# Kernel optimization log

Measured on AMD Instinct MI355X. Metric: run time of the kernel, lower is better.

The kernel has to match this reference:

```python
import jax, jax.numpy as jnp
import numpy as np

LN_EPS = 1e-12  # BERT LayerNorm eps


def _lstm_dir(x, wih, whh, bih, bhh, reverse):
    # x: [T, B, D] -> outputs [T, B, Hd]; torch gate order i, f, g, o
    B = x.shape[1]
    Hd = whh.shape[1]
    b = bih + bhh

    def step(carry, xt):
        h, c = carry
        gates = xt @ wih.T + h @ whh.T + b  # [B, 4*Hd]
        i, f, g, o = jnp.split(gates, 4, axis=-1)
        c = jax.nn.sigmoid(f) * c + jax.nn.sigmoid(i) * jnp.tanh(g)
        h = jax.nn.sigmoid(o) * jnp.tanh(c)
        return (h, c), h

    init = (jnp.zeros((B, Hd), x.dtype), jnp.zeros((B, Hd), x.dtype))
    _, ys = jax.lax.scan(step, init, x, reverse=reverse)
    return ys


def _forward(input_ids, labels, word_emb, pos_emb, type_emb, ln_g, ln_b,
             w_ih, w_hh, b_ih, b_hh, fc_w, fc_b, crf_start, crf_end, crf_trans):
    B, T = input_ids.shape
    # BERT embeddings (eval mode: dropout = identity)
    emb = word_emb[input_ids] + pos_emb[:T][None, :, :] + type_emb[0][None, None, :]
    mu = emb.mean(-1, keepdims=True)
    var = ((emb - mu) ** 2).mean(-1, keepdims=True)
    emb = (emb - mu) / jnp.sqrt(var + LN_EPS) * ln_g + ln_b

    # stacked bidirectional LSTM
    x = emb.transpose(1, 0, 2)  # [T, B, 768]
    n_layers = w_ih.shape[0]
    for l in range(n_layers):
        f = _lstm_dir(x, w_ih[l, 0], w_hh[l, 0], b_ih[l, 0], b_hh[l, 0], False)
        r = _lstm_dir(x, w_ih[l, 1], w_hh[l, 1], b_ih[l, 1], b_hh[l, 1], True)
        x = jnp.concatenate([f, r], axis=-1)  # [T, B, 768]
    out = x.transpose(1, 0, 2)  # [B, T, 768]

    em = out @ fc_w.T + fc_b  # emissions [B, T, C]

    # CRF log-likelihood (full mask, torchcrf reduction='sum')
    gold_em = jnp.take_along_axis(em, labels[..., None], axis=2)[..., 0]  # [B, T]
    score = (crf_start[labels[:, 0]]
             + gold_em.sum(axis=1)
             + crf_trans[labels[:, :-1], labels[:, 1:]].sum(axis=1)
             + crf_end[labels[:, -1]])

    alpha0 = crf_start[None, :] + em[:, 0]  # [B, C]

    def step(alpha, e_t):
        a = jax.nn.logsumexp(alpha[:, :, None] + crf_trans[None, :, :], axis=1) + e_t
        return a, None

    alpha, _ = jax.lax.scan(step, alpha0, em[:, 1:].transpose(1, 0, 2))
    logZ = jax.nn.logsumexp(alpha + crf_end[None, :], axis=1)  # [B]
    return jnp.sum(logZ - score)  # loss = -llh


def setup_inputs() -> dict:
    key = jax.random.key(0)
    ks = jax.random.split(key, 16)
    B, T, V, P, D, C, L, Hd = 32, 256, 30522, 512, 768, 14, 2, 384
    s = 0.05
    return {
        "input_ids": jax.random.randint(ks[0], (B, T), 0, V),
        "labels": jax.random.randint(ks[1], (B, T), 0, C),
        "word_emb": jax.random.normal(ks[2], (V, D), jnp.float32) * 0.02,
        "pos_emb": jax.random.normal(ks[3], (P, D), jnp.float32) * 0.02,
        "type_emb": jax.random.normal(ks[4], (2, D), jnp.float32) * 0.02,
        "ln_g": jnp.ones((D,), jnp.float32),
        "ln_b": jnp.zeros((D,), jnp.float32),
        "w_ih": jax.random.normal(ks[5], (L, 2, 4 * Hd, D), jnp.float32) * s,
        "w_hh": jax.random.normal(ks[6], (L, 2, 4 * Hd, Hd), jnp.float32) * s,
        "b_ih": jax.random.normal(ks[7], (L, 2, 4 * Hd), jnp.float32) * s,
        "b_hh": jax.random.normal(ks[8], (L, 2, 4 * Hd), jnp.float32) * s,
        "fc_w": jax.random.normal(ks[9], (C, D), jnp.float32) * s,
        "fc_b": jnp.zeros((C,), jnp.float32),
        "crf_start": jax.random.normal(ks[10], (C,), jnp.float32) * 0.1,
        "crf_end": jax.random.normal(ks[11], (C,), jnp.float32) * 0.1,
        "crf_trans": jax.random.normal(ks[12], (C, C), jnp.float32) * 0.1,
    }


def reference(input_ids, labels, word_emb, pos_emb, type_emb, ln_g, ln_b,
              w_ih, w_hh, b_ih, b_hh, fc_w, fc_b, crf_start, crf_end, crf_trans):
    return _forward(input_ids, labels, word_emb, pos_emb, type_emb, ln_g, ln_b,
                    w_ih, w_hh, b_ih, b_hh, fc_w, fc_b, crf_start, crf_end, crf_trans)
```

## Files before the change

### kernel.cpp

```cpp
#include <hip/hip_runtime.h>

typedef unsigned short u16;
typedef unsigned long long u64;
typedef __bf16 bfx8 __attribute__((ext_vector_type(8)));
typedef float  fx4  __attribute__((ext_vector_type(4)));

static __device__ __forceinline__ float b2f(u16 u){
  unsigned v = ((unsigned)u) << 16;
  return __builtin_bit_cast(float, v);
}
static __device__ __forceinline__ u16 f2b(float f){
  unsigned u = __builtin_bit_cast(unsigned, f);
  u = (u + 0x7FFFu + ((u >> 16) & 1u)) >> 16;
  return (u16)u;
}
static __device__ __forceinline__ float blo(unsigned v){ return b2f((u16)(v & 0xFFFFu)); }
static __device__ __forceinline__ float bhi(unsigned v){ return b2f((u16)(v >> 16)); }
static __device__ __forceinline__ float sigm(float x){
  float cx = fminf(fmaxf(x, -30.f), 30.f);
  float e = __expf(-cx);
  return __builtin_amdgcn_rcpf(1.f + e);
}
static __device__ __forceinline__ float tanh_f(float x){
  float cx = fminf(fmaxf(x, -15.f), 15.f);
  float e = __expf(2.f * cx);
  return (e - 1.f) * __builtin_amdgcn_rcpf(e + 1.f);
}
static __device__ __forceinline__ u64 ald64(const u64* p){
  return __hip_atomic_load(p, __ATOMIC_RELAXED, __HIP_MEMORY_SCOPE_AGENT);
}
static __device__ __forceinline__ void ast64(u64* p, u64 v){
  __hip_atomic_store(p, v, __ATOMIC_RELAXED, __HIP_MEMORY_SCOPE_AGENT);
}

__global__ __launch_bounds__(256) void embed_ln(
    const int* __restrict__ ids, const float* __restrict__ we,
    const float* __restrict__ pe, const float* __restrict__ te,
    const float* __restrict__ lng, const float* __restrict__ lnb,
    u16* __restrict__ X)
{
  int row = blockIdx.x;
  int t = row >> 5, b = row & 31;
  int id = ids[b * 256 + t];
  int tid = threadIdx.x;
  int wv = tid >> 6, lane = tid & 63;
  __shared__ float red[8];
  float v[3]; float s = 0.f, s2 = 0.f;
  const float* wrow = we + (long)id * 768;
  const float* prow = pe + (long)t * 768;
#pragma unroll
  for (int u = 0; u < 3; ++u){
    int k = tid + 256 * u;
    float x = wrow[k] + prow[k] + te[k];
    v[u] = x; s += x; s2 += x * x;
  }
#pragma unroll
  for (int o = 32; o > 0; o >>= 1){ s += __shfl_xor(s, o); s2 += __shfl_xor(s2, o); }
  if (lane == 0){ red[wv] = s; red[4 + wv] = s2; }
  __syncthreads();
  float S  = red[0] + red[1] + red[2] + red[3];
  float S2 = red[4] + red[5] + red[6] + red[7];
  float mu = S * (1.f / 768.f);
  float var = S2 * (1.f / 768.f) - mu * mu;
  float rs = rsqrtf(var + 1e-12f);
#pragma unroll
  for (int u = 0; u < 3; ++u){
    int k = tid + 256 * u;
    float y = (v[u] - mu) * rs * lng[k] + lnb[k];
    X[(long)row * 768 + k] = f2b(y);
  }
}

__global__ __launch_bounds__(256) void gemm_pre(
    const u16* __restrict__ A,
    const float* __restrict__ W,
    const float* __restrict__ bi,
    const float* __restrict__ bh,
    u16* __restrict__ pre)
{
  __shared__ u16 la[64][40];
  __shared__ u16 lb[64][40];
  int m0 = blockIdx.x * 64, n0 = blockIdx.y * 64;
  int tid = threadIdx.x;
  int wv = tid >> 6, lane = tid & 63;
  int l15 = lane & 15, l4 = lane >> 4;
  int r = tid >> 2, seg = (tid & 3) * 8;
  fx4 acc[4];
#pragma unroll
  for (int i = 0; i < 4; ++i){ acc[i][0]=0.f; acc[i][1]=0.f; acc[i][2]=0.f; acc[i][3]=0.f; }
  for (int k0 = 0; k0 < 768; k0 += 32){
    __syncthreads();
    *reinterpret_cast<uint4*>(&la[r][seg]) =
        *reinterpret_cast<const uint4*>(&A[(long)(m0 + r) * 768 + k0 + seg]);
    {
      const float* src = &W[(long)(n0 + r) * 768 + k0 + seg];
      union { u16 h[8]; uint4 v; } tb;
#pragma unroll
      for (int e = 0; e < 8; ++e) tb.h[e] = f2b(src[e]);
      *reinterpret_cast<uint4*>(&lb[r][seg]) = tb.v;
    }
    __syncthreads();
    bfx8 af = __builtin_bit_cast(bfx8, *reinterpret_cast<const uint4*>(&la[wv * 16 + l15][8 * l4]));
#pragma unroll
    for (int nt = 0; nt < 4; ++nt){
      bfx8 bf = __builtin_bit_cast(bfx8, *reinterpret_cast<const uint4*>(&lb[nt * 16 + l15][8 * l4]));
      acc[nt] = __builtin_amdgcn_mfma_f32_16x16x32_bf16(af, bf, acc[nt], 0, 0, 0);
    }
  }
#pragma unroll
  for (int nt = 0; nt < 4; ++nt){
    int n = n0 + nt * 16 + l15;
    int d = (n >= 1536) ? 1 : 0;
    int np = n - d * 1536;
    float bias = bi[n] + bh[n];
#pragma unroll
    for (int q = 0; q < 4; ++q){
      int m = m0 + wv * 16 + 4 * l4 + q;
      int tt = m >> 5, bb = m & 31;
      float vv = acc[nt][q] + bias;
      pre[((long)((d * 256 + tt) * 32 + bb)) * 1536 + np] = f2b(vv);
    }
  }
}

__global__ __launch_bounds__(256) void lstm_layer(
    const float* __restrict__ Whh,
    const u16*  __restrict__ pre,
    u16* __restrict__ Y,
    u64* __restrict__ H64)
{
  __shared__ u16 lw[64][386];
  __shared__ u16 hb[32][386];
  __shared__ float gl2[4][16][33];
  int wg = blockIdx.x;
  int d = wg / 24, sl = wg - d * 24;
  int js = sl * 16;
  int tid = threadIdx.x;
  int wv = tid >> 6, lane = tid & 63;
  int l15 = lane & 15, l4 = lane >> 4;
  int b0 = tid & 31, q = tid >> 5;
  int jl0 = 2 * q, jl1 = 2 * q + 1;

  ast64(&H64[((long)(1 * 2 + d) * 192 + sl * 8 + q) * 32 + b0], 0ull);
  u64 own_word = 0ull;

  for (int i = tid; i < 64 * 96; i += 256){
    int rr = i / 96, c4 = i - rr * 96;
    const float* src = Whh + ((long)(d * 1536 + (rr >> 4) * 384 + js + (rr & 15))) * 384 + 4 * c4;
    float4 v = *reinterpret_cast<const float4*>(src);
    short4 pk;
    pk.x = (short)f2b(v.x); pk.y = (short)f2b(v.y);
    pk.z = (short)f2b(v.z); pk.w = (short)f2b(v.w);
    *reinterpret_cast<short4*>(&lw[rr][(4 * c4) ^ (8 * (rr & 7))]) = pk;
  }
  __syncthreads();

  float c0 = 0.f, c1 = 0.f;

  int t0 = d ? 255 : 0;
  int t1 = d ? 254 : 1;
  const u16* pb0 = pre + ((long)(d * 256 + t0) * 32 + b0) * 1536 + js + jl0;
  const u16* pb1 = pre + ((long)(d * 256 + t1) * 32 + b0) * 1536 + js + jl0;
  uint4 pc, pn;
  pc.x = *reinterpret_cast<const unsigned*>(pb0 + 0 * 384);
  pc.y = *reinterpret_cast<const unsigned*>(pb0 + 1 * 384);
  pc.z = *reinterpret_cast<const unsigned*>(pb0 + 2 * 384);
  pc.w = *reinterpret_cast<const unsigned*>(pb0 + 3 * 384);
  pn.x = *reinterpret_cast<const unsigned*>(pb1 + 0 * 384);
  pn.y = *reinterpret_cast<const unsigned*>(pb1 + 1 * 384);
  pn.z = *reinterpret_cast<const unsigned*>(pb1 + 2 * 384);
  pn.w = *reinterpret_cast<const unsigned*>(pb1 + 3 * 384);

  for (int s = 0; s < 256; ++s){
    int tt = d ? (255 - s) : s;
    int pr = (s + 1) & 1;
    int pw = s & 1;

    {
      const u64* hsrc = H64 + (long)(pr * 2 + d) * 192 * 32;
      unsigned tagv = (unsigned)s;
      __builtin_amdgcn_s_sleep(2);
      for (;;){
        u64 vb[24];
#pragma unroll
        for (int i = 0; i < 24; ++i) vb[i] = ald64(&hsrc[tid + 256 * i]);
#pragma unroll
        for (int i = 0; i < 24; ++i) if (i == sl) vb[i] = own_word;
        bool ok = true;
#pragma unroll
        for (int i = 0; i < 24; ++i) ok = ok && ((unsigned)(vb[i] >> 32) == tagv);
#pragma unroll
        for (int i = 0; i < 24; ++i){
          int f = tid + 256 * i;
          int bb = f & 31, j2 = f >> 5;
          *reinterpret_cast<unsigned*>(&hb[bb][(2 * j2) ^ (8 * (bb & 7))]) = (unsigned)vb[i];
        }
        if (__syncthreads_and((int)ok)) break;
      }
    }

    int s2 = (s + 2 < 256) ? (s + 2) : 255;
    int t2 = d ? (255 - s2) : s2;
    const u16* pb2 = pre + ((long)(d * 256 + t2) * 32 + b0) * 1536 + js + jl0;
    uint4 p2;
    p2.x = *reinterpret_cast<const unsigned*>(pb2 + 0 * 384);
    p2.y = *reinterpret_cast<const unsigned*>(pb2 + 1 * 384);
    p2.z = *reinterpret_cast<const unsigned*>(pb2 + 2 * 384);
    p2.w = *reinterpret_cast<const unsigned*>(pb2 + 3 * 384);

    fx4 a0a, a0b, a1a, a1b;
#pragma unroll
    for (int z = 0; z < 4; ++z){ a0a[z]=0.f; a0b[z]=0.f; a1a[z]=0.f; a1b[z]=0.f; }
#pragma unroll
    for (int kk = 0; kk < 12; kk += 2){
      int col0 = (kk * 32 + 8 * l4) ^ (8 * (l15 & 7));
      int col1 = ((kk + 1) * 32 + 8 * l4) ^ (8 * (l15 & 7));
      bfx8 bw0 = __builtin_bit_cast(bfx8, *reinterpret_cast<const uint4*>(&lw[wv * 16 + l15][col0]));
      bfx8 h00 = __builtin_bit_cast(bfx8, *reinterpret_cast<const uint4*>(&hb[l15][col0]));
      bfx8 h10 = __builtin_bit_cast(bfx8, *reinterpret_cast<const uint4*>(&hb[16 + l15][col0]));
      bfx8 bw1 = __builtin_bit_cast(bfx8, *reinterpret_cast<const uint4*>(&lw[wv * 16 + l15][col1]));
      bfx8 h01 = __builtin_bit_cast(bfx8, *reinterpret_cast<const uint4*>(&hb[l15][col1]));
      bfx8 h11 = __builtin_bit_cast(bfx8, *reinterpret_cast<const uint4*>(&hb[16 + l15][col1]));
      a0a = __builtin_amdgcn_mfma_f32_16x16x32_bf16(h00, bw0, a0a, 0, 0, 0);
      a1a = __builtin_amdgcn_mfma_f32_16x16x32_bf16(h10, bw0, a1a, 0, 0, 0);
      a0b = __builtin_amdgcn_mfma_f32_16x16x32_bf16(h01, bw1, a0b, 0, 0, 0);
      a1b = __builtin_amdgcn_mfma_f32_16x16x32_bf16(h11, bw1, a1b, 0, 0, 0);
    }
#pragma unroll
    for (int qq = 0; qq < 4; ++qq){
      int bb0 = (4 * l4 + qq) ^ (4 * (l15 & 7));
      int bb1 = (16 + 4 * l4 + qq) ^ (4 * (l15 & 7));
      gl2[wv][l15][bb0] = a0a[qq] + a0b[qq];
      gl2[wv][l15][bb1] = a1a[qq] + a1b[qq];
    }
    __syncthreads();

    int x0 = b0 ^ (4 * (jl0 & 7));
    int x1 = b0 ^ (4 * (jl1 & 7));
    float gi0 = gl2[0][jl0][x0] + blo(pc.x), gi1 = gl2[0][jl1][x1] + bhi(pc.x);
    float gf0 = gl2[1][jl0][x0] + blo(pc.y), gf1 = gl2[1][jl1][x1] + bhi(pc.y);
    float gg0 = gl2[2][jl0][x0] + blo(pc.z), gg1 = gl2[2][jl1][x1] + bhi(pc.z);
    float go0 = gl2[3][jl0][x0] + blo(pc.w), go1 = gl2[3][jl1][x1] + bhi(pc.w);
    c0 = sigm(gf0) * c0 + sigm(gi0) * tanh_f(gg0);
    float h0 = sigm(go0) * tanh_f(c0);
    c1 = sigm(gf1) * c1 + sigm(gi1) * tanh_f(gg1);
    float h1 = sigm(go1) * tanh_f(c1);

    unsigned hv = (unsigned)f2b(h0) | ((unsigned)f2b(h1) << 16);
    own_word = ((u64)(unsigned)(s + 1) << 32) | (u64)hv;
    ast64(&H64[((long)(pw * 2 + d) * 192 + sl * 8 + q) * 32 + b0], own_word);
    *reinterpret_cast<unsigned*>(&Y[((long)tt * 32 + b0) * 768 + d * 384 + js + jl0]) = hv;
    pc = pn; pn = p2;
  }
}

__global__ __launch_bounds__(256) void fc_em(
    const u16* __restrict__ Y2, const float* __restrict__ fw,
    const float* __restrict__ fb, float* __restrict__ em)
{
  int row = blockIdx.x * 4 + (threadIdx.x >> 6);
  int lane = threadIdx.x & 63;
  float acc[14];
#pragma unroll
  for (int c = 0; c < 14; ++c) acc[c] = 0.f;
#pragma unroll
  for (int u = 0; u < 12; ++u){
    int k = lane + 64 * u;
    float y = b2f(Y2[(long)row * 768 + k]);
#pragma unroll
    for (int c = 0; c < 14; ++c) acc[c] += y * fw[c * 768 + k];
  }
#pragma unroll
  for (int c = 0; c < 14; ++c){
    float a = acc[c];
#pragma unroll
    for (int o = 32; o > 0; o >>= 1) a += __shfl_xor(a, o);
    acc[c] = a;
  }
  if (lane == 0){
    int tt = row >> 5, b = row & 31;
#pragma unroll
    for (int c = 0; c < 14; ++c) em[(long)(b * 256 + tt) * 14 + c] = acc[c] + fb[c];
  }
}

__global__ __launch_bounds__(64) void crf_fwd(
    const float* __restrict__ em,
    const int* __restrict__ labels,
    const float* __restrict__ cs, const float* __restrict__ ce,
    const float* __restrict__ ct,
    float* __restrict__ lossb)
{
  int b = blockIdx.x;
  int lane = threadIdx.x;
  const float* E = em + (long)b * 256 * 14;
  const int* L = labels + b * 256;

  float sc = 0.f;
  for (int t = lane; t < 256; t += 64){
    int lt = L[t];
    sc += E[t * 14 + lt];
    if (t < 255) sc += ct[lt * 14 + L[t + 1]];
  }
#pragma unroll
  for (int o = 32; o > 0; o >>= 1) sc += __shfl_xor(sc, o);
  float score = sc + cs[L[0]] + ce[L[255]];

  __shared__ float al[2][16];
  int j = lane >> 2, ih = lane & 3;
  if (lane < 16){
    al[0][lane] = (lane < 14) ? (cs[lane] + E[lane]) : -1e30f;
    al[1][lane] = -1e30f;
  }
  __syncthreads();
  float tr[4];
#pragma unroll
  for (int w = 0; w < 4; ++w){
    int i = ih * 4 + w;
    tr[w] = (i < 14 && j < 14) ? ct[i * 14 + j] : -1e30f;
  }
  for (int t = 1; t < 256; ++t){
    int par = t & 1;
    float vals[4]; float m = -1e30f;
#pragma unroll
    for (int w = 0; w < 4; ++w){
      int i = ih * 4 + w;
      float v = al[par ^ 1][i] + tr[w];
      vals[w] = v; m = fmaxf(m, v);
    }
    m = fmaxf(m, __shfl_xor(m, 1));
    m = fmaxf(m, __shfl_xor(m, 2));
    float s = 0.f;
#pragma unroll
    for (int w = 0; w < 4; ++w) s += __expf(vals[w] - m);
    s += __shfl_xor(s, 1);
    s += __shfl_xor(s, 2);
    if (ih == 0 && j < 14) al[par][j] = m + __logf(s) + E[t * 14 + j];
    __syncthreads();
  }
  float v = (lane < 14) ? (al[1][lane] + ce[lane]) : -1e30f;
  float mm = v;
#pragma unroll
  for (int o = 32; o > 0; o >>= 1) mm = fmaxf(mm, __shfl_xor(mm, o));
  float ss = (lane < 14) ? __expf(v - mm) : 0.f;
#pragma unroll
  for (int o = 32; o > 0; o >>= 1) ss += __shfl_xor(ss, o);
  if (lane == 0) lossb[b] = (mm + __logf(ss)) - score;
}

__global__ __launch_bounds__(64) void final_sum(const float* __restrict__ lb, float* __restrict__ out){
  int lane = threadIdx.x;
  float v = (lane < 32) ? lb[lane] : 0.f;
#pragma unroll
  for (int o = 32; o > 0; o >>= 1) v += __shfl_xor(v, o);
  if (lane == 0) out[0] = v;
}

extern "C" void kernel_launch(void* const* d_in, const int* in_sizes, int n_in,
                              void* d_out, int out_size, void* d_ws, size_t ws_size,
                              hipStream_t stream)
{
  const int*   ids = (const int*)d_in[0];
  const int*   lab = (const int*)d_in[1];
  const float* we  = (const float*)d_in[2];
  const float* pe  = (const float*)d_in[3];
  const float* te  = (const float*)d_in[4];
  const float* lng = (const float*)d_in[5];
  const float* lnb = (const float*)d_in[6];
  const float* wih = (const float*)d_in[7];
  const float* whh = (const float*)d_in[8];
  const float* bih = (const float*)d_in[9];
  const float* bhh = (const float*)d_in[10];
  const float* fcw = (const float*)d_in[11];
  const float* fcb = (const float*)d_in[12];
  const float* cs  = (const float*)d_in[13];
  const float* ce  = (const float*)d_in[14];
  const float* ct  = (const float*)d_in[15];
  float* out = (float*)d_out;

  char* ws = (char*)d_ws;
  size_t off = 0;
  u16* X0  = (u16*)(ws + off); off += (size_t)8192 * 768 * 2;
  u16* Y1  = (u16*)(ws + off); off += (size_t)8192 * 768 * 2;
  u16* PRE = (u16*)(ws + off); off += (size_t)2 * 256 * 32 * 1536 * 2;
  float* EM = (float*)(ws + off); off += (size_t)32 * 256 * 14 * 4;
  u64* H64a = (u64*)(ws + off); off += (size_t)2 * 2 * 192 * 32 * 8;
  u64* H64b = (u64*)(ws + off); off += (size_t)2 * 2 * 192 * 32 * 8;
  float* LB = (float*)(ws + off); off += 128;
  u16* Y2 = X0;

  embed_ln<<<8192, 256, 0, stream>>>(ids, we, pe, te, lng, lnb, X0);

  gemm_pre<<<dim3(128, 48), 256, 0, stream>>>(X0, wih, bih, bhh, PRE);
  lstm_layer<<<48, 256, 0, stream>>>(whh, PRE, Y1, H64a);
  gemm_pre<<<dim3(128, 48), 256, 0, stream>>>(Y1, wih + (size_t)2 * 1536 * 768,
                                              bih + 2 * 1536, bhh + 2 * 1536, PRE);
  lstm_layer<<<48, 256, 0, stream>>>(whh + (size_t)2 * 1536 * 384, PRE, Y2, H64b);

  fc_em<<<2048, 256, 0, stream>>>(Y2, fcw, fcb, EM);
  crf_fwd<<<32, 64, 0, stream>>>(EM, lab, cs, ce, ct, LB);
  final_sum<<<1, 64, 0, stream>>>(LB, out);
}
```

Baseline: 2.439 ms.

## Replace tagged 64-bit hidden-state polling with per-workgroup progress counters

Cross-workgroup synchronisation in the persistent LSTM kernel used to poll all 24 tagged 64-bit hidden-state words per thread until every tag matched. It now polls 24 per-workgroup progress counters (one per slice) and then loads the 32-bit hidden values once. Each producer drains its stores with a waitcnt and a barrier before bumping its counter. This shrinks polling traffic and the data width, but it adds an extra barrier and a store drain to every step and relies on relaxed atomics being ordered correctly by the waitcnt.

```diff
diff --git a/kernel.cpp b/kernel.cpp
--- a/kernel.cpp
+++ b/kernel.cpp
@@ -1,7 +1,6 @@
 #include <hip/hip_runtime.h>
 
 typedef unsigned short u16;
-typedef unsigned long long u64;
 typedef __bf16 bfx8 __attribute__((ext_vector_type(8)));
 typedef float  fx4  __attribute__((ext_vector_type(4)));
 
@@ -26,10 +25,10 @@
   float e = __expf(2.f * cx);
   return (e - 1.f) * __builtin_amdgcn_rcpf(e + 1.f);
 }
-static __device__ __forceinline__ u64 ald64(const u64* p){
+static __device__ __forceinline__ unsigned ald32(const unsigned* p){
   return __hip_atomic_load(p, __ATOMIC_RELAXED, __HIP_MEMORY_SCOPE_AGENT);
 }
-static __device__ __forceinline__ void ast64(u64* p, u64 v){
+static __device__ __forceinline__ void ast32(unsigned* p, unsigned v){
   __hip_atomic_store(p, v, __ATOMIC_RELAXED, __HIP_MEMORY_SCOPE_AGENT);
 }
 
@@ -123,11 +122,16 @@
   }
 }
 
+__global__ void zero_can(unsigned* __restrict__ c, int n){
+  if ((int)threadIdx.x < n) c[threadIdx.x] = 0u;
+}
+
 __global__ __launch_bounds__(256) void lstm_layer(
     const float* __restrict__ Whh,
     const u16*  __restrict__ pre,
     u16* __restrict__ Y,
-    u64* __restrict__ H64)
+    unsigned* __restrict__ H32,
+    unsigned* __restrict__ CAN)
 {
   __shared__ u16 lw[64][386];
   __shared__ u16 hb[32][386];
@@ -141,8 +145,10 @@
   int b0 = tid & 31, q = tid >> 5;
   int jl0 = 2 * q, jl1 = 2 * q + 1;
 
-  ast64(&H64[((long)(1 * 2 + d) * 192 + sl * 8 + q) * 32 + b0], 0ull);
-  u64 own_word = 0ull;
+  ast32(&H32[((long)(1 * 2 + d) * 192 + sl * 8 + q) * 32 + b0], 0u);
+  asm volatile("s_waitcnt vmcnt(0)" ::: "memory");
+  __syncthreads();
+  if (tid == 0) ast32(&CAN[d * 24 + sl], 1u);
 
   for (int i = tid; i < 64 * 96; i += 256){
     int rr = i / 96, c4 = i - rr * 96;
@@ -171,32 +177,36 @@
   pn.z = *reinterpret_cast<const unsigned*>(pb1 + 2 * 384);
   pn.w = *reinterpret_cast<const unsigned*>(pb1 + 3 * 384);
 
+  const unsigned* cn = CAN + d * 24;
+  bool poller = (tid < 24);
+
   for (int s = 0; s < 256; ++s){
     int tt = d ? (255 - s) : s;
     int pr = (s + 1) & 1;
     int pw = s & 1;
 
     {
-      const u64* hsrc = H64 + (long)(pr * 2 + d) * 192 * 32;
-      unsigned tagv = (unsigned)s;
-      __builtin_amdgcn_s_sleep(2);
+      unsigned need = (unsigned)(s + 1);
       for (;;){
-        u64 vb[24];
-#pragma unroll
-        for (int i = 0; i < 24; ++i) vb[i] = ald64(&hsrc[tid + 256 * i]);
-#pragma unroll
-        for (int i = 0; i < 24; ++i) if (i == sl) vb[i] = own_word;
         bool ok = true;
-#pragma unroll
-        for (int i = 0; i < 24; ++i) ok = ok && ((unsigned)(vb[i] >> 32) == tagv);
-#pragma unroll
-        for (int i = 0; i < 24; ++i){
-          int f = tid + 256 * i;
-          int bb = f & 31, j2 = f >> 5;
-          *reinterpret_cast<unsigned*>(&hb[bb][(2 * j2) ^ (8 * (bb & 7))]) = (unsigned)vb[i];
-        }
+        if (poller) ok = (ald32(&cn[tid]) >= need);
         if (__syncthreads_and((int)ok)) break;
+        __builtin_amdgcn_s_sleep(1);
       }
+    }
+
+    {
+      const unsigned* hsrc = H32 + (long)(pr * 2 + d) * 192 * 32;
+      unsigned vb[24];
+#pragma unroll
+      for (int i = 0; i < 24; ++i) vb[i] = ald32(&hsrc[tid + 256 * i]);
+#pragma unroll
+      for (int i = 0; i < 24; ++i){
+        int f = tid + 256 * i;
+        int bb = f & 31, j2 = f >> 5;
+        *reinterpret_cast<unsigned*>(&hb[bb][(2 * j2) ^ (8 * (bb & 7))]) = vb[i];
+      }
+      __syncthreads();
     }
 
     int s2 = (s + 2 < 256) ? (s + 2) : 255;
@@ -247,9 +257,11 @@
     float h1 = sigm(go1) * tanh_f(c1);
 
     unsigned hv = (unsigned)f2b(h0) | ((unsigned)f2b(h1) << 16);
-    own_word = ((u64)(unsigned)(s + 1) << 32) | (u64)hv;
-    ast64(&H64[((long)(pw * 2 + d) * 192 + sl * 8 + q) * 32 + b0], own_word);
+    ast32(&H32[((long)(pw * 2 + d) * 192 + sl * 8 + q) * 32 + b0], hv);
     *reinterpret_cast<unsigned*>(&Y[((long)tt * 32 + b0) * 768 + d * 384 + js + jl0]) = hv;
+    asm volatile("s_waitcnt vmcnt(0)" ::: "memory");
+    __syncthreads();
+    if (tid == 0) ast32(&CAN[d * 24 + sl], (unsigned)(s + 2));
     pc = pn; pn = p2;
   }
 }
@@ -384,18 +396,22 @@
   u16* Y1  = (u16*)(ws + off); off += (size_t)8192 * 768 * 2;
   u16* PRE = (u16*)(ws + off); off += (size_t)2 * 256 * 32 * 1536 * 2;
   float* EM = (float*)(ws + off); off += (size_t)32 * 256 * 14 * 4;
-  u64* H64a = (u64*)(ws + off); off += (size_t)2 * 2 * 192 * 32 * 8;
-  u64* H64b = (u64*)(ws + off); off += (size_t)2 * 2 * 192 * 32 * 8;
+  unsigned* H32a = (unsigned*)(ws + off); off += (size_t)2 * 2 * 192 * 32 * 4;
+  unsigned* H32b = (unsigned*)(ws + off); off += (size_t)2 * 2 * 192 * 32 * 4;
+  unsigned* CANa = (unsigned*)(ws + off); off += 256;
+  unsigned* CANb = (unsigned*)(ws + off); off += 256;
   float* LB = (float*)(ws + off); off += 128;
   u16* Y2 = X0;
 
+  zero_can<<<1, 64, 0, stream>>>(CANa, 48);
+  zero_can<<<1, 64, 0, stream>>>(CANb, 48);
   embed_ln<<<8192, 256, 0, stream>>>(ids, we, pe, te, lng, lnb, X0);
 
   gemm_pre<<<dim3(128, 48), 256, 0, stream>>>(X0, wih, bih, bhh, PRE);
-  lstm_layer<<<48, 256, 0, stream>>>(whh, PRE, Y1, H64a);
+  lstm_layer<<<48, 256, 0, stream>>>(whh, PRE, Y1, H32a, CANa);
   gemm_pre<<<dim3(128, 48), 256, 0, stream>>>(Y1, wih + (size_t)2 * 1536 * 768,
                                               bih + 2 * 1536, bhh + 2 * 1536, PRE);
-  lstm_layer<<<48, 256, 0, stream>>>(whh + (size_t)2 * 1536 * 384, PRE, Y2, H64b);
+  lstm_layer<<<48, 256, 0, stream>>>(whh + (size_t)2 * 1536 * 384, PRE, Y2, H32b, CANb);
 
   fc_em<<<2048, 256, 0, stream>>>(Y2, fcw, fcb, EM);
   crf_fwd<<<32, 64, 0, stream>>>(EM, lab, cs, ce, ct, LB);
```

After: 2.462 ms. No clear change (+0.9%).

## Interleave both LSTM directions within each workgroup, halving the persistent grid

Applied to the files above, without the earlier changes.

Each lstm_layer workgroup now holds both directions' recurrent weight slices in LDS and alternates forward and reverse substeps, so the grid drops from 48 to 24 workgroups. While one direction's tagged hidden-state words are still in flight, the workgroup can do the other direction's work, hiding the cross-workgroup spin-wait latency. The s_sleep and the own-word substitution are dropped. The cost is doubled serial compute per workgroup and more LDS per block.

```diff
diff --git a/kernel.cpp b/kernel.cpp
--- a/kernel.cpp
+++ b/kernel.cpp
@@ -123,134 +123,157 @@
   }
 }
 
+template<int D>
+static __device__ __forceinline__ void substep(
+    int s, int tid, int sl, int js, int wv, int l15, int l4, int b0, int q, int jl0,
+    const u16* __restrict__ pre, u16* __restrict__ Y, u64* __restrict__ H64,
+    u16 (*lwD)[386], u16 (*hb)[386], float (*gl2)[16][33],
+    float& c0, float& c1, uint4& pc, uint4& pn)
+{
+  int tt = D ? (255 - s) : s;
+  int pr = (s + 1) & 1;
+  int pw = s & 1;
+
+  {
+    const u64* hsrc = H64 + (long)(pr * 2 + D) * 192 * 32;
+    unsigned tagv = (unsigned)s;
+    for (;;){
+      u64 vb[24];
+#pragma unroll
+      for (int i = 0; i < 24; ++i) vb[i] = ald64(&hsrc[tid + 256 * i]);
+      bool ok = true;
+#pragma unroll
+      for (int i = 0; i < 24; ++i) ok = ok && ((unsigned)(vb[i] >> 32) == tagv);
+#pragma unroll
+      for (int i = 0; i < 24; ++i){
+        int f = tid + 256 * i;
+        int bb = f & 31, j2 = f >> 5;
+        *reinterpret_cast<unsigned*>(&hb[bb][(2 * j2) ^ (8 * (bb & 7))]) = (unsigned)vb[i];
+      }
+      if (__syncthreads_and((int)ok)) break;
+    }
+  }
+
+  int s2 = (s + 2 < 256) ? (s + 2) : 255;
+  int t2 = D ? (255 - s2) : s2;
+  const u16* pb2 = pre + ((long)(D * 256 + t2) * 32 + b0) * 1536 + js + jl0;
+  uint4 p2;
+  p2.x = *reinterpret_cast<const unsigned*>(pb2 + 0 * 384);
+  p2.y = *reinterpret_cast<const unsigned*>(pb2 + 1 * 384);
+  p2.z = *reinterpret_cast<const unsigned*>(pb2 + 2 * 384);
+  p2.w = *reinterpret_cast<const unsigned*>(pb2 + 3 * 384);
+
+  fx4 a0a, a0b, a1a, a1b;
+#pragma unroll
+  for (int z = 0; z < 4; ++z){ a0a[z]=0.f; a0b[z]=0.f; a1a[z]=0.f; a1b[z]=0.f; }
+#pragma unroll
+  for (int kk = 0; kk < 12; kk += 2){
+    int col0 = (kk * 32 + 8 * l4) ^ (8 * (l15 & 7));
+    int col1 = ((kk + 1) * 32 + 8 * l4) ^ (8 * (l15 & 7));
+    bfx8 bw0 = __builtin_bit_cast(bfx8, *reinterpret_cast<const uint4*>(&lwD[wv * 16 + l15][col0]));
+    bfx8 h00 = __builtin_bit_cast(bfx8, *reinterpret_cast<const uint4*>(&hb[l15][col0]));
+    bfx8 h10 = __builtin_bit_cast(bfx8, *reinterpret_cast<const uint4*>(&hb[16 + l15][col0]));
+    bfx8 bw1 = __builtin_bit_cast(bfx8, *reinterpret_cast<const uint4*>(&lwD[wv * 16 + l15][col1]));
+    bfx8 h01 = __builtin_bit_cast(bfx8, *reinterpret_cast<const uint4*>(&hb[l15][col1]));
+    bfx8 h11 = __builtin_bit_cast(bfx8, *reinterpret_cast<const uint4*>(&hb[16 + l15][col1]));
+    a0a = __builtin_amdgcn_mfma_f32_16x16x32_bf16(h00, bw0, a0a, 0, 0, 0);
+    a1a = __builtin_amdgcn_mfma_f32_16x16x32_bf16(h10, bw0, a1a, 0, 0, 0);
+    a0b = __builtin_amdgcn_mfma_f32_16x16x32_bf16(h01, bw1, a0b, 0, 0, 0);
+    a1b = __builtin_amdgcn_mfma_f32_16x16x32_bf16(h11, bw1, a1b, 0, 0, 0);
+  }
+#pragma unroll
+  for (int qq = 0; qq < 4; ++qq){
+    int bb0 = (4 * l4 + qq) ^ (4 * (l15 & 7));
+    int bb1 = (16 + 4 * l4 + qq) ^ (4 * (l15 & 7));
+    gl2[wv][l15][bb0] = a0a[qq] + a0b[qq];
+    gl2[wv][l15][bb1] = a1a[qq] + a1b[qq];
+  }
+  __syncthreads();
+
+  int jl1 = jl0 + 1;
+  int x0 = b0 ^ (4 * (jl0 & 7));
+  int x1 = b0 ^ (4 * (jl1 & 7));
+  float gi0 = gl2[0][jl0][x0] + blo(pc.x), gi1 = gl2[0][jl1][x1] + bhi(pc.x);
+  float gf0 = gl2[1][jl0][x0] + blo(pc.y), gf1 = gl2[1][jl1][x1] + bhi(pc.y);
+  float gg0 = gl2[2][jl0][x0] + blo(pc.z), gg1 = gl2[2][jl1][x1] + bhi(pc.z);
+  float go0 = gl2[3][jl0][x0] + blo(pc.w), go1 = gl2[3][jl1][x1] + bhi(pc.w);
+  c0 = sigm(gf0) * c0 + sigm(gi0) * tanh_f(gg0);
+  float h0 = sigm(go0) * tanh_f(c0);
+  c1 = sigm(gf1) * c1 + sigm(gi1) * tanh_f(gg1);
+  float h1 = sigm(go1) * tanh_f(c1);
+
+  unsigned hv = (unsigned)f2b(h0) | ((unsigned)f2b(h1) << 16);
+  ast64(&H64[((long)(pw * 2 + D) * 192 + sl * 8 + q) * 32 + b0],
+        ((u64)(unsigned)(s + 1) << 32) | (u64)hv);
+  *reinterpret_cast<unsigned*>(&Y[((long)tt * 32 + b0) * 768 + D * 384 + js + jl0]) = hv;
+  pc = pn; pn = p2;
+}
+
 __global__ __launch_bounds__(256) void lstm_layer(
     const float* __restrict__ Whh,
     const u16*  __restrict__ pre,
     u16* __restrict__ Y,
     u64* __restrict__ H64)
 {
-  __shared__ u16 lw[64][386];
+  __shared__ u16 lw[2][64][386];
   __shared__ u16 hb[32][386];
   __shared__ float gl2[4][16][33];
-  int wg = blockIdx.x;
-  int d = wg / 24, sl = wg - d * 24;
+  int sl = blockIdx.x;
   int js = sl * 16;
   int tid = threadIdx.x;
   int wv = tid >> 6, lane = tid & 63;
   int l15 = lane & 15, l4 = lane >> 4;
   int b0 = tid & 31, q = tid >> 5;
-  int jl0 = 2 * q, jl1 = 2 * q + 1;
-
-  ast64(&H64[((long)(1 * 2 + d) * 192 + sl * 8 + q) * 32 + b0], 0ull);
-  u64 own_word = 0ull;
-
-  for (int i = tid; i < 64 * 96; i += 256){
-    int rr = i / 96, c4 = i - rr * 96;
-    const float* src = Whh + ((long)(d * 1536 + (rr >> 4) * 384 + js + (rr & 15))) * 384 + 4 * c4;
+  int jl0 = 2 * q;
+
+  ast64(&H64[((long)(1 * 2 + 0) * 192 + sl * 8 + q) * 32 + b0], 0ull);
+  ast64(&H64[((long)(1 * 2 + 1) * 192 + sl * 8 + q) * 32 + b0], 0ull);
+
+  for (int i = tid; i < 2 * 64 * 96; i += 256){
+    int dd = i / (64 * 96);
+    int rem = i - dd * 64 * 96;
+    int rr = rem / 96, c4 = rem - rr * 96;
+    const float* src = Whh + ((long)(dd * 1536 + (rr >> 4) * 384 + js + (rr & 15))) * 384 + 4 * c4;
     float4 v = *reinterpret_cast<const float4*>(src);
     short4 pk;
     pk.x = (short)f2b(v.x); pk.y = (short)f2b(v.y);
     pk.z = (short)f2b(v.z); pk.w = (short)f2b(v.w);
-    *reinterpret_cast<short4*>(&lw[rr][(4 * c4) ^ (8 * (rr & 7))]) = pk;
+    *reinterpret_cast<short4*>(&lw[dd][rr][(4 * c4) ^ (8 * (rr & 7))]) = pk;
   }
   __syncthreads();
 
-  float c0 = 0.f, c1 = 0.f;
-
-  int t0 = d ? 255 : 0;
-  int t1 = d ? 254 : 1;
-  const u16* pb0 = pre + ((long)(d * 256 + t0) * 32 + b0) * 1536 + js + jl0;
-  const u16* pb1 = pre + ((long)(d * 256 + t1) * 32 + b0) * 1536 + js + jl0;
-  uint4 pc, pn;
-  pc.x = *reinterpret_cast<const unsigned*>(pb0 + 0 * 384);
-  pc.y = *reinterpret_cast<const unsigned*>(pb0 + 1 * 384);
-  pc.z = *reinterpret_cast<const unsigned*>(pb0 + 2 * 384);
-  pc.w = *reinterpret_cast<const unsigned*>(pb0 + 3 * 384);
-  pn.x = *reinterpret_cast<const unsigned*>(pb1 + 0 * 384);
-  pn.y = *reinterpret_cast<const unsigned*>(pb1 + 1 * 384);
-  pn.z = *reinterpret_cast<const unsigned*>(pb1 + 2 * 384);
-  pn.w = *reinterpret_cast<const unsigned*>(pb1 + 3 * 384);
+  float c00 = 0.f, c01 = 0.f;
+  float c10 = 0.f, c11 = 0.f;
+
+  uint4 pc0, pn0, pc1, pn1;
+  {
+    const u16* p00 = pre + ((long)(0 * 256 + 0)   * 32 + b0) * 1536 + js + jl0;
+    const u16* p01 = pre + ((long)(0 * 256 + 1)   * 32 + b0) * 1536 + js + jl0;
+    const u16* p10 = pre + ((long)(1 * 256 + 255) * 32 + b0) * 1536 + js + jl0;
+    const u16* p11 = pre + ((long)(1 * 256 + 254) * 32 + b0) * 1536 + js + jl0;
+    pc0.x = *reinterpret_cast<const unsigned*>(p00 + 0 * 384);
+    pc0.y = *reinterpret_cast<const unsigned*>(p00 + 1 * 384);
+    pc0.z = *reinterpret_cast<const unsigned*>(p00 + 2 * 384);
+    pc0.w = *reinterpret_cast<const unsigned*>(p00 + 3 * 384);
+    pn0.x = *reinterpret_cast<const unsigned*>(p01 + 0 * 384);
+    pn0.y = *reinterpret_cast<const unsigned*>(p01 + 1 * 384);
+    pn0.z = *reinterpret_cast<const unsigned*>(p01 + 2 * 384);
+    pn0.w = *reinterpret_cast<const unsigned*>(p01 + 3 * 384);
+    pc1.x = *reinterpret_cast<const unsigned*>(p10 + 0 * 384);
+    pc1.y = *reinterpret_cast<const unsigned*>(p10 + 1 * 384);
+    pc1.z = *reinterpret_cast<const unsigned*>(p10 + 2 * 384);
+    pc1.w = *reinterpret_cast<const unsigned*>(p10 + 3 * 384);
+    pn1.x = *reinterpret_cast<const unsigned*>(p11 + 0 * 384);
+    pn1.y = *reinterpret_cast<const unsigned*>(p11 + 1 * 384);
+    pn1.z = *reinterpret_cast<const unsigned*>(p11 + 2 * 384);
+    pn1.w = *reinterpret_cast<const unsigned*>(p11 + 3 * 384);
+  }
 
   for (int s = 0; s < 256; ++s){
-    int tt = d ? (255 - s) : s;
-    int pr = (s + 1) & 1;
-    int pw = s & 1;
-
-    {
-      const u64* hsrc = H64 + (long)(pr * 2 + d) * 192 * 32;
-      unsigned tagv = (unsigned)s;
-      __builtin_amdgcn_s_sleep(2);
-      for (;;){
-        u64 vb[24];
-#pragma unroll
-        for (int i = 0; i < 24; ++i) vb[i] = ald64(&hsrc[tid + 256 * i]);
-#pragma unroll
-        for (int i = 0; i < 24; ++i) if (i == sl) vb[i] = own_word;
-        bool ok = true;
-#pragma unroll
-        for (int i = 0; i < 24; ++i) ok = ok && ((unsigned)(vb[i] >> 32) == tagv);
-#pragma unroll
-        for (int i = 0; i < 24; ++i){
-          int f = tid + 256 * i;
-          int bb = f & 31, j2 = f >> 5;
-          *reinterpret_cast<unsigned*>(&hb[bb][(2 * j2) ^ (8 * (bb & 7))]) = (unsigned)vb[i];
-        }
-        if (__syncthreads_and((int)ok)) break;
-      }
-    }
-
-    int s2 = (s + 2 < 256) ? (s + 2) : 255;
-    int t2 = d ? (255 - s2) : s2;
-    const u16* pb2 = pre + ((long)(d * 256 + t2) * 32 + b0) * 1536 + js + jl0;
-    uint4 p2;
-    p2.x = *reinterpret_cast<const unsigned*>(pb2 + 0 * 384);
-    p2.y = *reinterpret_cast<const unsigned*>(pb2 + 1 * 384);
-    p2.z = *reinterpret_cast<const unsigned*>(pb2 + 2 * 384);
-    p2.w = *reinterpret_cast<const unsigned*>(pb2 + 3 * 384);
-
-    fx4 a0a, a0b, a1a, a1b;
-#pragma unroll
-    for (int z = 0; z < 4; ++z){ a0a[z]=0.f; a0b[z]=0.f; a1a[z]=0.f; a1b[z]=0.f; }
-#pragma unroll
-    for (int kk = 0; kk < 12; kk += 2){
-      int col0 = (kk * 32 + 8 * l4) ^ (8 * (l15 & 7));
-      int col1 = ((kk + 1) * 32 + 8 * l4) ^ (8 * (l15 & 7));
-      bfx8 bw0 = __builtin_bit_cast(bfx8, *reinterpret_cast<const uint4*>(&lw[wv * 16 + l15][col0]));
-      bfx8 h00 = __builtin_bit_cast(bfx8, *reinterpret_cast<const uint4*>(&hb[l15][col0]));
-      bfx8 h10 = __builtin_bit_cast(bfx8, *reinterpret_cast<const uint4*>(&hb[16 + l15][col0]));
-      bfx8 bw1 = __builtin_bit_cast(bfx8, *reinterpret_cast<const uint4*>(&lw[wv * 16 + l15][col1]));
-      bfx8 h01 = __builtin_bit_cast(bfx8, *reinterpret_cast<const uint4*>(&hb[l15][col1]));
-      bfx8 h11 = __builtin_bit_cast(bfx8, *reinterpret_cast<const uint4*>(&hb[16 + l15][col1]));
-      a0a = __builtin_amdgcn_mfma_f32_16x16x32_bf16(h00, bw0, a0a, 0, 0, 0);
-      a1a = __builtin_amdgcn_mfma_f32_16x16x32_bf16(h10, bw0, a1a, 0, 0, 0);
-      a0b = __builtin_amdgcn_mfma_f32_16x16x32_bf16(h01, bw1, a0b, 0, 0, 0);
-      a1b = __builtin_amdgcn_mfma_f32_16x16x32_bf16(h11, bw1, a1b, 0, 0, 0);
-    }
-#pragma unroll
-    for (int qq = 0; qq < 4; ++qq){
-      int bb0 = (4 * l4 + qq) ^ (4 * (l15 & 7));
-      int bb1 = (16 + 4 * l4 + qq) ^ (4 * (l15 & 7));
-      gl2[wv][l15][bb0] = a0a[qq] + a0b[qq];
-      gl2[wv][l15][bb1] = a1a[qq] + a1b[qq];
-    }
-    __syncthreads();
-
-    int x0 = b0 ^ (4 * (jl0 & 7));
-    int x1 = b0 ^ (4 * (jl1 & 7));
-    float gi0 = gl2[0][jl0][x0] + blo(pc.x), gi1 = gl2[0][jl1][x1] + bhi(pc.x);
-    float gf0 = gl2[1][jl0][x0] + blo(pc.y), gf1 = gl2[1][jl1][x1] + bhi(pc.y);
-    float gg0 = gl2[2][jl0][x0] + blo(pc.z), gg1 = gl2[2][jl1][x1] + bhi(pc.z);
-    float go0 = gl2[3][jl0][x0] + blo(pc.w), go1 = gl2[3][jl1][x1] + bhi(pc.w);
-    c0 = sigm(gf0) * c0 + sigm(gi0) * tanh_f(gg0);
-    float h0 = sigm(go0) * tanh_f(c0);
-    c1 = sigm(gf1) * c1 + sigm(gi1) * tanh_f(gg1);
-    float h1 = sigm(go1) * tanh_f(c1);
-
-    unsigned hv = (unsigned)f2b(h0) | ((unsigned)f2b(h1) << 16);
-    own_word = ((u64)(unsigned)(s + 1) << 32) | (u64)hv;
-    ast64(&H64[((long)(pw * 2 + d) * 192 + sl * 8 + q) * 32 + b0], own_word);
-    *reinterpret_cast<unsigned*>(&Y[((long)tt * 32 + b0) * 768 + d * 384 + js + jl0]) = hv;
-    pc = pn; pn = p2;
+    substep<0>(s, tid, sl, js, wv, l15, l4, b0, q, jl0,
+               pre, Y, H64, lw[0], hb, gl2, c00, c01, pc0, pn0);
+    substep<1>(s, tid, sl, js, wv, l15, l4, b0, q, jl0,
+               pre, Y, H64, lw[1], hb, gl2, c10, c11, pc1, pn1);
   }
 }
 
@@ -392,10 +415,10 @@
   embed_ln<<<8192, 256, 0, stream>>>(ids, we, pe, te, lng, lnb, X0);
 
   gemm_pre<<<dim3(128, 48), 256, 0, stream>>>(X0, wih, bih, bhh, PRE);
-  lstm_layer<<<48, 256, 0, stream>>>(whh, PRE, Y1, H64a);
+  lstm_layer<<<24, 256, 0, stream>>>(whh, PRE, Y1, H64a);
   gemm_pre<<<dim3(128, 48), 256, 0, stream>>>(Y1, wih + (size_t)2 * 1536 * 768,
                                               bih + 2 * 1536, bhh + 2 * 1536, PRE);
-  lstm_layer<<<48, 256, 0, stream>>>(whh + (size_t)2 * 1536 * 384, PRE, Y2, H64b);
+  lstm_layer<<<24, 256, 0, stream>>>(whh + (size_t)2 * 1536 * 384, PRE, Y2, H64b);
 
   fc_em<<<2048, 256, 0, stream>>>(Y2, fcw, fcb, EM);
   crf_fwd<<<32, 64, 0, stream>>>(EM, lab, cs, ce, ct, LB);
```

Measured after the change: 6.523 ms. +167.4%, slower.
